# Performance work log

Measured on AMD Instinct MI355X. Metric: run time of the kernel, lower is better.

The kernel has to match this reference:

```python
import jax, jax.numpy as jnp
import numpy as np

N_NODES = 50000
N_EDGES = 640000
RAW = 128
HID = 256
COORD = 3


def setup_inputs() -> dict:
    key = jax.random.key(0)
    ks = jax.random.split(key, 20)

    def w(k, fan_in, fan_out):
        return (jax.random.normal(k, (fan_in, fan_out), jnp.float32)
                / np.float32(np.sqrt(fan_in)))

    return {
        "edge_index": jax.random.randint(ks[0], (2, N_EDGES), 0, N_NODES, jnp.int64)
        if jax.config.jax_enable_x64 else
        jax.random.randint(ks[0], (2, N_EDGES), 0, N_NODES, jnp.int32),
        "str_feature": jax.random.normal(ks[1], (N_NODES, RAW), jnp.float32),
        "coord_feature": jax.random.normal(ks[2], (N_NODES, COORD), jnp.float32),
        # msg_mlp: Linear(2*RAW+1 -> HID), SiLU, Linear(HID -> HID), SiLU
        "msg_w1": w(ks[3], 2 * RAW + 1, HID), "msg_b1": jnp.zeros((HID,), jnp.float32),
        "msg_w2": w(ks[4], HID, HID), "msg_b2": jnp.zeros((HID,), jnp.float32),
        # trans_mlp: Linear(HID->HID), SiLU, Linear(HID->HID), SiLU, Linear(HID->1, no bias, xavier gain=0.001)
        "tr_w1": w(ks[5], HID, HID), "tr_b1": jnp.zeros((HID,), jnp.float32),
        "tr_w2": w(ks[6], HID, HID), "tr_b2": jnp.zeros((HID,), jnp.float32),
        "tr_w3": w(ks[7], HID, 1) * np.float32(0.001),
        # posi_mlp: Linear(RAW+HID->HID), SiLU, Linear(HID->RAW)
        "posi_w1": w(ks[8], RAW + HID, HID), "posi_b1": jnp.zeros((HID,), jnp.float32),
        "posi_w2": w(ks[9], HID, RAW), "posi_b2": jnp.zeros((RAW,), jnp.float32),
    }


def reference(edge_index, str_feature, coord_feature,
              msg_w1, msg_b1, msg_w2, msg_b2,
              tr_w1, tr_b1, tr_w2, tr_b2, tr_w3,
              posi_w1, posi_b1, posi_w2, posi_b2):
    silu = jax.nn.silu
    row, col = edge_index[0], edge_index[1]
    n = str_feature.shape[0]

    # coord2dist
    coord_diff = coord_feature[row] - coord_feature[col]          # [E, 3]
    sqr_dist = jnp.sum(coord_diff * coord_diff, axis=1, keepdims=True)  # [E, 1]

    # msg_model
    edge_in = jnp.concatenate([str_feature[row], str_feature[col], sqr_dist], axis=1)
    msg = silu(silu(edge_in @ msg_w1 + msg_b1) @ msg_w2 + msg_b2)  # [E, HID]

    # coord_model: trans = coord_diff * trans_mlp(msg); x += segment_mean(trans, row)
    gate = silu(silu(msg @ tr_w1 + tr_b1) @ tr_w2 + tr_b2) @ tr_w3  # [E, 1]
    trans = coord_diff * gate                                       # [E, 3]
    trans_sum = jax.ops.segment_sum(trans, row, num_segments=n)     # [N, 3]
    cnt = jax.ops.segment_sum(jnp.ones((trans.shape[0],), trans.dtype), row,
                              num_segments=n)
    trans_mean = trans_sum / jnp.clip(cnt, 1.0)[:, None]
    coord_out = coord_feature + trans_mean

    # posi_model: p + posi_mlp([p, segment_sum(msg, row)])
    msg_sum = jax.ops.segment_sum(msg, row, num_segments=n)         # [N, HID]
    p_in = jnp.concatenate([str_feature, msg_sum], axis=1)
    str_out = str_feature + (silu(p_in @ posi_w1 + posi_b1) @ posi_w2 + posi_b2)

    return str_out, coord_out
```

## Files before the change

kernel.cpp:

```cpp
#include <hip/hip_runtime.h>

#define NN 50000
#define NE 640000

typedef __bf16 bf16x8 __attribute__((ext_vector_type(8)));
typedef short  short8 __attribute__((ext_vector_type(8)));
typedef float  f32x16 __attribute__((ext_vector_type(16)));
typedef float  f32x2  __attribute__((ext_vector_type(2)));
typedef float  f32x4  __attribute__((ext_vector_type(4)));

__device__ __forceinline__ short f2bf(float v) {
  unsigned u = __builtin_bit_cast(unsigned, v);
  u = (u + 0x7FFFu + ((u >> 16) & 1u)) >> 16;
  return (short)u;
}
__device__ __forceinline__ short f2bf_hw(float v) {
  return __builtin_bit_cast(short, (__bf16)v);
}
__device__ __forceinline__ unsigned pack2(float a, float b) {
  return (unsigned)(unsigned short)f2bf_hw(a) | ((unsigned)(unsigned short)f2bf_hw(b) << 16);
}
__device__ __forceinline__ float silu_f(float v) {
  float e = __builtin_amdgcn_exp2f(v * -1.44269504f);
  return v * __builtin_amdgcn_rcpf(1.0f + e);
}
__device__ __forceinline__ bf16x8 ld8(const short* p) {
  return *(const bf16x8*)(p);
}
__device__ __forceinline__ void atomic_add_f(float* p, float v) {
  __hip_atomic_fetch_add(p, v, __ATOMIC_RELAXED, __HIP_MEMORY_SCOPE_AGENT);
}

__global__ void egcl_prep(const float* __restrict__ mw1, const float* __restrict__ mb1,
                          const float* __restrict__ mw2, const float* __restrict__ mb2,
                          const float* __restrict__ tw1, const float* __restrict__ tb1,
                          const float* __restrict__ tw2, const float* __restrict__ tb2,
                          const float* __restrict__ pw1, const float* __restrict__ pw2,
                          const float* __restrict__ strf, const int* __restrict__ rowp,
                          short* __restrict__ w1t, short* __restrict__ w2t,
                          short* __restrict__ t1t, short* __restrict__ t2t,
                          short* __restrict__ p1t, short* __restrict__ p2t,
                          short* __restrict__ strb, int* __restrict__ deg)
{
  const int S0 = 71680, S2 = 98304, S3 = 32768, SS = NN * 128;
  const int total = 4 * S0 + S2 + S3 + SS + NE;
  int stride = gridDim.x * blockDim.x;
  for (int i = blockIdx.x * blockDim.x + threadIdx.x; i < total; i += stride) {
    int j = i;
    if (j < S0) { int n = j / 280, k = j - n * 280;
      float v = (k < 257) ? mw1[k * 256 + n] : ((k == 257) ? mb1[n] : 0.0f);
      w1t[j] = f2bf(v); continue; }
    j -= S0;
    if (j < S0) { int n = j / 280, k = j - n * 280;
      float v = (k < 256) ? mw2[k * 256 + n] : ((k == 257) ? mb2[n] : 0.0f);
      w2t[j] = f2bf(v); continue; }
    j -= S0;
    if (j < S0) { int n = j / 280, k = j - n * 280;
      float v = (k < 256) ? tw1[k * 256 + n] : ((k == 257) ? tb1[n] : 0.0f);
      t1t[j] = f2bf(v); continue; }
    j -= S0;
    if (j < S0) { int n = j / 280, k = j - n * 280;
      float v = (k < 256) ? tw2[k * 256 + n] : ((k == 257) ? tb2[n] : 0.0f);
      t2t[j] = f2bf(v); continue; }
    j -= S0;
    if (j < S2) { int n = j / 384, k = j - n * 384; p1t[j] = f2bf(pw1[k * 256 + n]); continue; }
    j -= S2;
    if (j < S3) { int n = j >> 8, k = j & 255; p2t[j] = f2bf(pw2[k * 128 + n]); continue; }
    j -= S3;
    if (j < SS) { strb[j] = f2bf(strf[j]); continue; }
    j -= SS;
    atomicAdd(deg + rowp[j], 1);
  }
}

__global__ __launch_bounds__(1024)
void egcl_scan(const int* __restrict__ deg, int* __restrict__ base)
{
  __shared__ int wsum[16], wincl[16];
  __shared__ int carry_s;
  const int tid = threadIdx.x, lane = tid & 63, w = tid >> 6;
  if (tid == 0) carry_s = 0;
  __syncthreads();
  for (int start = 0; start < NN; start += 1024) {
    const int i = start + tid;
    int v = (i < NN) ? deg[i] : 0;
    int s = v;
#pragma unroll
    for (int off = 1; off < 64; off <<= 1) {
      int t = __shfl_up(s, off);
      if (lane >= off) s += t;
    }
    if (lane == 63) wsum[w] = s;
    __syncthreads();
    if (w == 0) {
      int u = (lane < 16) ? wsum[lane] : 0;
#pragma unroll
      for (int off = 1; off < 16; off <<= 1) {
        int t = __shfl_up(u, off);
        if (lane >= off) u += t;
      }
      if (lane < 16) wincl[lane] = u;
    }
    __syncthreads();
    const int waveoff = wincl[w] - wsum[w];
    const int carry = carry_s;
    if (i < NN) base[i] = carry + waveoff + s - v;
    __syncthreads();
    if (tid == 0) carry_s = carry + wincl[15];
    __syncthreads();
  }
  if (tid == 0) base[NN] = NE;
}

__global__ void egcl_scatter(const int* __restrict__ rowp, const int* __restrict__ base,
                             int* __restrict__ cursor, int* __restrict__ eidg)
{
  int stride = gridDim.x * blockDim.x;
  for (int e = blockIdx.x * blockDim.x + threadIdx.x; e < NE; e += stride) {
    int r = rowp[e];
    int pos = base[r] + atomicAdd(cursor + r, 1);
    eidg[pos] = e;
  }
}


__device__ __forceinline__ void gemm32(const short* Ab, const short* __restrict__ WT,
                                       int wn, int nh, int lh, int l32,
                                       f32x16 acc[2])
{
  acc[0] = (f32x16)(0.0f); acc[1] = (f32x16)(0.0f);
  const short* arow = Ab + l32 * 280 + lh * 8;
  const short* brow = WT + (wn * 64 + nh * 32 + l32) * 280 + lh * 8;
#pragma unroll
  for (int ks = 0; ks < 17; ++ks) {
    const int kb = ks * 16;
    bf16x8 b  = ld8(brow + kb);
    bf16x8 a0 = ld8(arow + kb);
    bf16x8 a1 = ld8(arow + 32 * 280 + kb);
    acc[0] = __builtin_amdgcn_mfma_f32_32x32x16_bf16(a0, b, acc[0], 0, 0, 0);
    acc[1] = __builtin_amdgcn_mfma_f32_32x32x16_bf16(a1, b, acc[1], 0, 0, 0);
  }
}

__device__ __forceinline__ void comp_pack32(const f32x16 acc[2], unsigned pk[16])
{
#pragma unroll
  for (int sm = 0; sm < 2; ++sm)
#pragma unroll
    for (int j = 0; j < 8; ++j) {
      float v0 = silu_f(acc[sm][2 * j]);
      float v1 = silu_f(acc[sm][2 * j + 1]);
      pk[sm * 8 + j] = pack2(v0, v1);
    }
}

__device__ __forceinline__ void write_pk32(short* Ab, const unsigned pk0[16],
                                           const unsigned pk1[16],
                                           int wn, int lh, int l32)
{
#pragma unroll
  for (int nh = 0; nh < 2; ++nh) {
    const unsigned* pk = nh ? pk1 : pk0;
    const int n = wn * 64 + nh * 32 + l32;
#pragma unroll
    for (int sm = 0; sm < 2; ++sm) {
      short* dst = Ab + (sm * 32 + 4 * lh) * 280 + n;
#pragma unroll
      for (int j = 0; j < 8; ++j) {
        const int row = (j & 1) * 2 + 8 * (j >> 1);
        const unsigned u = pk[sm * 8 + j];
        dst[row * 280]       = (short)(u & 0xFFFFu);
        dst[(row + 1) * 280] = (short)(u >> 16);
      }
    }
  }
}

__global__ __launch_bounds__(256, 4)
void egcl_edge(const int* __restrict__ eidx, const float* __restrict__ coord,
               const short* __restrict__ strb, const int* __restrict__ eidg,
               const int* __restrict__ base,
               const short* __restrict__ w1t, const short* __restrict__ w2t,
               const short* __restrict__ t1t, const short* __restrict__ t2t,
               const float* __restrict__ tr_w3,
               float* __restrict__ msg_sum, float* __restrict__ trans_sum)
{
  __shared__ short Ab[64 * 280];
  __shared__ int   rs_s[64], cs_s[64], own_s[64];
  __shared__ float cdx_s[64], cdy_s[64], cdz_s[64], gate_s[64];

  const int tid  = threadIdx.x;
  const int lane = tid & 63, wave = tid >> 6;
  const int lh = lane >> 5, l32 = lane & 31;
  const int wn = wave;
  const int p0 = blockIdx.x * 64;
  const int* __restrict__ rowp = eidx;
  const int* __restrict__ colp = eidx + NE;

  if (tid < 64) {
    int e = eidg[p0 + tid];
    int r = rowp[e], c = colp[e];
    rs_s[tid] = r; cs_s[tid] = c;
    const int wstart = p0 + (tid & ~31);
    own_s[tid] = (base[r] >= wstart) && (base[r + 1] <= wstart + 32) ? 1 : 0;
    float dx = coord[r * 3 + 0] - coord[c * 3 + 0];
    float dy = coord[r * 3 + 1] - coord[c * 3 + 1];
    float dz = coord[r * 3 + 2] - coord[c * 3 + 2];
    cdx_s[tid] = dx; cdy_s[tid] = dy; cdz_s[tid] = dz;
    short8 d8 = (short8)(short)0;
    d8[0] = f2bf(dx * dx + dy * dy + dz * dz);
    d8[1] = f2bf(1.0f);
    *(short8*)(Ab + tid * 280 + 256) = d8;
    *(short8*)(Ab + tid * 280 + 264) = (short8)(short)0;
    *(short8*)(Ab + tid * 280 + 272) = (short8)(short)0;
  }
  __syncthreads();
#pragma unroll
  for (int it = 0; it < 8; ++it) {
    int i = tid + it * 256;
    int e = i >> 5, cc = i & 31;
    int node = (cc < 16) ? rs_s[e] : cs_s[e];
    short8 v = *(const short8*)(strb + node * 128 + (cc & 15) * 8);
    *(short8*)(Ab + e * 280 + cc * 8) = v;
  }
  __syncthreads();

  f32x16 acc[2];
  unsigned pk0[16], pk1[16];

  gemm32(Ab, w1t, wn, 0, lh, l32, acc);
  comp_pack32(acc, pk0);
  gemm32(Ab, w1t, wn, 1, lh, l32, acc);
  comp_pack32(acc, pk1);
  __syncthreads();
  write_pk32(Ab, pk0, pk1, wn, lh, l32);
  __syncthreads();

  gemm32(Ab, w2t, wn, 0, lh, l32, acc);
  comp_pack32(acc, pk0);
  gemm32(Ab, w2t, wn, 1, lh, l32, acc);
  comp_pack32(acc, pk1);
  __syncthreads();
  write_pk32(Ab, pk0, pk1, wn, lh, l32);
  __syncthreads();

  gemm32(Ab, t1t, wn, 0, lh, l32, acc);
  comp_pack32(acc, pk0);
  gemm32(Ab, t1t, wn, 1, lh, l32, acc);
  comp_pack32(acc, pk1);
  {
    const int cp  = tid & 127;
    const int e0w = (tid >> 7) * 32;
    float run0 = 0.0f, run1 = 0.0f;
    int prev = rs_s[e0w];
    int own  = own_s[e0w];
#pragma unroll 4
    for (int i = 0; i < 32; ++i) {
      const int idx = e0w + i;
      const int r = rs_s[idx];
      unsigned u = *(const unsigned*)(Ab + idx * 280 + cp * 2);
      float lo = __builtin_bit_cast(float, u << 16);
      float hi = __builtin_bit_cast(float, u & 0xFFFF0000u);
      if (r != prev) {
        if (own) {
          f32x2 v; v.x = run0; v.y = run1;
          *((f32x2*)msg_sum + prev * 128 + cp) = v;
        } else {
          atomic_add_f(msg_sum + prev * 256 + cp * 2 + 0, run0);
          atomic_add_f(msg_sum + prev * 256 + cp * 2 + 1, run1);
        }
        run0 = 0.0f; run1 = 0.0f; prev = r; own = own_s[idx];
      }
      run0 += lo; run1 += hi;
    }
    if (own) {
      f32x2 v; v.x = run0; v.y = run1;
      *((f32x2*)msg_sum + prev * 128 + cp) = v;
    } else {
      atomic_add_f(msg_sum + prev * 256 + cp * 2 + 0, run0);
      atomic_add_f(msg_sum + prev * 256 + cp * 2 + 1, run1);
    }
  }
  __syncthreads();
  write_pk32(Ab, pk0, pk1, wn, lh, l32);
  __syncthreads();

  gemm32(Ab, t2t, wn, 0, lh, l32, acc);
  comp_pack32(acc, pk0);
  gemm32(Ab, t2t, wn, 1, lh, l32, acc);
  comp_pack32(acc, pk1);
  __syncthreads();
  write_pk32(Ab, pk0, pk1, wn, lh, l32);
  __syncthreads();

  {
    const int e = tid >> 2, p = tid & 3;
    const short* ap = Ab + e * 280 + p * 64;
    const float4* wp = (const float4*)(tr_w3 + p * 64);
    float s = 0.0f;
#pragma unroll
    for (int j = 0; j < 8; ++j) {
      bf16x8 av = ld8(ap + j * 8);
      float4 w0 = wp[2 * j], w1 = wp[2 * j + 1];
      s += (float)av[0] * w0.x + (float)av[1] * w0.y + (float)av[2] * w0.z + (float)av[3] * w0.w;
      s += (float)av[4] * w1.x + (float)av[5] * w1.y + (float)av[6] * w1.z + (float)av[7] * w1.w;
    }
    s += __shfl_xor(s, 1);
    s += __shfl_xor(s, 2);
    if (p == 0) gate_s[e] = s;
  }
  __syncthreads();
  if (tid < 3) {
    const int c = tid;
    float run = 0.0f;
    int prev = rs_s[0];
    for (int i = 0; i < 64; ++i) {
      const int r = rs_s[i];
      if (r != prev) { atomic_add_f(trans_sum + prev * 3 + c, run); run = 0.0f; prev = r; }
      const float cd = (c == 0) ? cdx_s[i] : ((c == 1) ? cdy_s[i] : cdz_s[i]);
      run += cd * gate_s[i];
    }
    atomic_add_f(trans_sum + prev * 3 + c, run);
  }
}

__global__ __launch_bounds__(256, 3)
void egcl_node(const float* __restrict__ strf, const float* __restrict__ coord,
               const short* __restrict__ strb,
               const short* __restrict__ p1t, const short* __restrict__ p2t,
               const float* __restrict__ pb1, const float* __restrict__ pb2,
               const float* __restrict__ msg_sum, const float* __restrict__ trans_sum,
               const int* __restrict__ base, float* __restrict__ out)
{
  __shared__ short Ab[64 * 392];
  const int tid  = threadIdx.x;
  const int lane = tid & 63, wave = tid >> 6;
  const int quad = lane >> 4, l16 = lane & 15;
  const int n0 = blockIdx.x * 64;

#pragma unroll
  for (int it = 0; it < 4; ++it) {
    int i = tid + it * 256;
    int m = i >> 4, c = i & 15;
    int n = n0 + m;
    short8 v = (short8)(short)0;
    if (n < NN) v = *(const short8*)(strb + n * 128 + c * 8);
    *(short8*)(Ab + m * 392 + c * 8) = v;
  }
#pragma unroll
  for (int it = 0; it < 8; ++it) {
    int i = tid + it * 256;
    int m = i >> 5, c = i & 31;
    int n = n0 + m;
    short8 v = (short8)(short)0;
    if (n < NN) {
      const float* src = msg_sum + n * 256 + c * 8;
#pragma unroll
      for (int j = 0; j < 8; ++j) v[j] = f2bf_hw(src[j]);
    }
    *(short8*)(Ab + m * 392 + 128 + c * 8) = v;
  }
  __syncthreads();

  f32x4 acc[4][4];
#pragma unroll
  for (int nt = 0; nt < 4; ++nt)
#pragma unroll
    for (int mt = 0; mt < 4; ++mt) acc[nt][mt] = (f32x4)(0.0f);
#pragma unroll
  for (int ks = 0; ks < 12; ++ks) {
    const int kb = ks * 32 + quad * 8;
    bf16x8 b[4];
#pragma unroll
    for (int nt = 0; nt < 4; ++nt)
      b[nt] = ld8(p1t + (wave * 64 + nt * 16 + l16) * 384 + kb);
#pragma unroll
    for (int mt = 0; mt < 4; ++mt) {
      bf16x8 a = ld8(Ab + (mt * 16 + l16) * 392 + kb);
#pragma unroll
      for (int nt = 0; nt < 4; ++nt)
        acc[nt][mt] = __builtin_amdgcn_mfma_f32_16x16x32_bf16(a, b[nt], acc[nt][mt], 0, 0, 0);
    }
  }
  __syncthreads();
#pragma unroll
  for (int nt = 0; nt < 4; ++nt) {
    const int n = wave * 64 + nt * 16 + l16;
    const float bn = pb1[n];
#pragma unroll
    for (int mt = 0; mt < 4; ++mt)
#pragma unroll
      for (int r = 0; r < 4; ++r) {
        const int m = mt * 16 + quad * 4 + r;
        Ab[m * 392 + n] = f2bf_hw(silu_f(acc[nt][mt][r] + bn));
      }
  }
  __syncthreads();

  f32x4 a2[2][4];
#pragma unroll
  for (int nt = 0; nt < 2; ++nt)
#pragma unroll
    for (int mt = 0; mt < 4; ++mt) a2[nt][mt] = (f32x4)(0.0f);
#pragma unroll
  for (int ks = 0; ks < 8; ++ks) {
    const int kb = ks * 32 + quad * 8;
    bf16x8 b0 = ld8(p2t + (wave * 32 + l16) * 256 + kb);
    bf16x8 b1 = ld8(p2t + (wave * 32 + 16 + l16) * 256 + kb);
#pragma unroll
    for (int mt = 0; mt < 4; ++mt) {
      bf16x8 a = ld8(Ab + (mt * 16 + l16) * 392 + kb);
      a2[0][mt] = __builtin_amdgcn_mfma_f32_16x16x32_bf16(a, b0, a2[0][mt], 0, 0, 0);
      a2[1][mt] = __builtin_amdgcn_mfma_f32_16x16x32_bf16(a, b1, a2[1][mt], 0, 0, 0);
    }
  }
#pragma unroll
  for (int nt = 0; nt < 2; ++nt) {
    const int c = wave * 32 + nt * 16 + l16;
    const float bc = pb2[c];
#pragma unroll
    for (int mt = 0; mt < 4; ++mt)
#pragma unroll
      for (int r = 0; r < 4; ++r) {
        const int m = mt * 16 + quad * 4 + r;
        const int n = n0 + m;
        if (n < NN) out[n * 128 + c] = strf[n * 128 + c] + a2[nt][mt][r] + bc;
      }
  }
  if (tid < 64) {
    const int n = n0 + tid;
    if (n < NN) {
      float cv = (float)(base[n + 1] - base[n]); if (cv < 1.0f) cv = 1.0f;
      float inv = __builtin_amdgcn_rcpf(cv);
      out[NN * 128 + n * 3 + 0] = coord[n * 3 + 0] + trans_sum[n * 3 + 0] * inv;
      out[NN * 128 + n * 3 + 1] = coord[n * 3 + 1] + trans_sum[n * 3 + 1] * inv;
      out[NN * 128 + n * 3 + 2] = coord[n * 3 + 2] + trans_sum[n * 3 + 2] * inv;
    }
  }
}

extern "C" void kernel_launch(void* const* d_in, const int* in_sizes, int n_in,
                              void* d_out, int out_size, void* d_ws, size_t ws_size,
                              hipStream_t stream)
{
  const int*   eidx   = (const int*)d_in[0];
  const float* strf   = (const float*)d_in[1];
  const float* coord  = (const float*)d_in[2];
  const float* msg_w1 = (const float*)d_in[3];
  const float* msg_b1 = (const float*)d_in[4];
  const float* msg_w2 = (const float*)d_in[5];
  const float* msg_b2 = (const float*)d_in[6];
  const float* tr_w1  = (const float*)d_in[7];
  const float* tr_b1  = (const float*)d_in[8];
  const float* tr_w2  = (const float*)d_in[9];
  const float* tr_b2  = (const float*)d_in[10];
  const float* tr_w3  = (const float*)d_in[11];
  const float* posi_w1 = (const float*)d_in[12];
  const float* posi_b1 = (const float*)d_in[13];
  const float* posi_w2 = (const float*)d_in[14];
  const float* posi_b2 = (const float*)d_in[15];
  float* out = (float*)d_out;

  char* ws = (char*)d_ws;
  float* msg_sum   = (float*)ws;
  float* trans_sum = msg_sum + NN * 256;
  int*   deg       = (int*)(trans_sum + NN * 3);
  int*   cursor    = deg + NN;
  int*   base      = cursor + NN;
  int*   eidg      = base + NN + 8;
  short* strb = (short*)(eidg + NE);
  short* w1t  = strb + NN * 128;
  short* w2t  = w1t + 71680;
  short* t1t  = w2t + 71680;
  short* t2t  = t1t + 71680;
  short* p1t  = t2t + 71680;
  short* p2t  = p1t + 98304;

  const int* rowp = eidx;

  (void)hipMemsetAsync(ws, 0, (size_t)(NN * 256 + NN * 3 + NN + NN) * 4, stream);
  egcl_prep<<<2048, 256, 0, stream>>>(msg_w1, msg_b1, msg_w2, msg_b2,
                                      tr_w1, tr_b1, tr_w2, tr_b2,
                                      posi_w1, posi_w2,
                                      strf, rowp, w1t, w2t, t1t, t2t, p1t, p2t, strb, deg);
  egcl_scan<<<1, 1024, 0, stream>>>(deg, base);
  egcl_scatter<<<2560, 256, 0, stream>>>(rowp, base, cursor, eidg);
  egcl_edge<<<NE / 64, 256, 0, stream>>>(eidx, coord, strb, eidg, base,
                                         w1t, w2t, t1t, t2t, tr_w3,
                                         msg_sum, trans_sum);
  egcl_node<<<(NN + 63) / 64, 256, 0, stream>>>(strf, coord, strb, p1t, p2t,
                                                posi_b1, posi_b2,
                                                msg_sum, trans_sum, base, out);
}
```

Baseline: 976.3 us.

## Compute full 64-column MFMA tiles per wave and fold biases into the epilogue

```diff
diff --git a/kernel.cpp b/kernel.cpp
--- a/kernel.cpp
+++ b/kernel.cpp
@@ -16,9 +16,6 @@
 }
 __device__ __forceinline__ short f2bf_hw(float v) {
   return __builtin_bit_cast(short, (__bf16)v);
-}
-__device__ __forceinline__ unsigned pack2(float a, float b) {
-  return (unsigned)(unsigned short)f2bf_hw(a) | ((unsigned)(unsigned short)f2bf_hw(b) << 16);
 }
 __device__ __forceinline__ float silu_f(float v) {
   float e = __builtin_amdgcn_exp2f(v * -1.44269504f);
@@ -124,53 +121,53 @@
 }
 
 
-__device__ __forceinline__ void gemm32(const short* Ab, const short* __restrict__ WT,
-                                       int wn, int nh, int lh, int l32,
-                                       f32x16 acc[2])
+template<int NKS>
+__device__ __forceinline__ void gemm64(const short* Ab, const short* __restrict__ WT,
+                                       int wn, int lh, int l32, f32x16 acc[4])
 {
   acc[0] = (f32x16)(0.0f); acc[1] = (f32x16)(0.0f);
+  acc[2] = (f32x16)(0.0f); acc[3] = (f32x16)(0.0f);
   const short* arow = Ab + l32 * 280 + lh * 8;
-  const short* brow = WT + (wn * 64 + nh * 32 + l32) * 280 + lh * 8;
-#pragma unroll
-  for (int ks = 0; ks < 17; ++ks) {
+  const short* brow = WT + (wn * 64 + l32) * 280 + lh * 8;
+#pragma unroll
+  for (int ks = 0; ks < NKS; ++ks) {
     const int kb = ks * 16;
-    bf16x8 b  = ld8(brow + kb);
+    bf16x8 b0 = ld8(brow + kb);
+    bf16x8 b1 = ld8(brow + 32 * 280 + kb);
     bf16x8 a0 = ld8(arow + kb);
     bf16x8 a1 = ld8(arow + 32 * 280 + kb);
-    acc[0] = __builtin_amdgcn_mfma_f32_32x32x16_bf16(a0, b, acc[0], 0, 0, 0);
-    acc[1] = __builtin_amdgcn_mfma_f32_32x32x16_bf16(a1, b, acc[1], 0, 0, 0);
-  }
-}
-
-__device__ __forceinline__ void comp_pack32(const f32x16 acc[2], unsigned pk[16])
-{
-#pragma unroll
-  for (int sm = 0; sm < 2; ++sm)
-#pragma unroll
-    for (int j = 0; j < 8; ++j) {
-      float v0 = silu_f(acc[sm][2 * j]);
-      float v1 = silu_f(acc[sm][2 * j + 1]);
-      pk[sm * 8 + j] = pack2(v0, v1);
-    }
-}
-
-__device__ __forceinline__ void write_pk32(short* Ab, const unsigned pk0[16],
-                                           const unsigned pk1[16],
-                                           int wn, int lh, int l32)
+    acc[0] = __builtin_amdgcn_mfma_f32_32x32x16_bf16(a0, b0, acc[0], 0, 0, 0);
+    acc[1] = __builtin_amdgcn_mfma_f32_32x32x16_bf16(a1, b0, acc[1], 0, 0, 0);
+    acc[2] = __builtin_amdgcn_mfma_f32_32x32x16_bf16(a0, b1, acc[2], 0, 0, 0);
+    acc[3] = __builtin_amdgcn_mfma_f32_32x32x16_bf16(a1, b1, acc[3], 0, 0, 0);
+  }
+}
+
+__device__ __forceinline__ void silu_acc(f32x16 acc[4], float b0, float b1)
+{
+#pragma unroll
+  for (int i = 0; i < 4; ++i) {
+    const float b = (i < 2) ? b0 : b1;
+#pragma unroll
+    for (int r = 0; r < 16; ++r) acc[i][r] = silu_f(acc[i][r] + b);
+  }
+}
+
+__device__ __forceinline__ void write_acc(short* Ab, const f32x16 acc[4],
+                                          int wn, int lh, int l32)
 {
 #pragma unroll
   for (int nh = 0; nh < 2; ++nh) {
-    const unsigned* pk = nh ? pk1 : pk0;
     const int n = wn * 64 + nh * 32 + l32;
 #pragma unroll
     for (int sm = 0; sm < 2; ++sm) {
+      const f32x16& a = acc[nh * 2 + sm];
       short* dst = Ab + (sm * 32 + 4 * lh) * 280 + n;
 #pragma unroll
       for (int j = 0; j < 8; ++j) {
         const int row = (j & 1) * 2 + 8 * (j >> 1);
-        const unsigned u = pk[sm * 8 + j];
-        dst[row * 280]       = (short)(u & 0xFFFFu);
-        dst[(row + 1) * 280] = (short)(u >> 16);
+        dst[row * 280]       = f2bf_hw(a[2 * j]);
+        dst[(row + 1) * 280] = f2bf_hw(a[2 * j + 1]);
       }
     }
   }
@@ -182,11 +179,13 @@
                const int* __restrict__ base,
                const short* __restrict__ w1t, const short* __restrict__ w2t,
                const short* __restrict__ t1t, const short* __restrict__ t2t,
+               const float* __restrict__ mb2v, const float* __restrict__ tb1v,
+               const float* __restrict__ tb2v,
                const float* __restrict__ tr_w3,
                float* __restrict__ msg_sum, float* __restrict__ trans_sum)
 {
   __shared__ short Ab[64 * 280];
-  __shared__ int   rs_s[64], cs_s[64], own_s[64];
+  __shared__ int   rs_s[64], own_s[64];
   __shared__ float cdx_s[64], cdy_s[64], cdz_s[64], gate_s[64];
 
   const int tid  = threadIdx.x;
@@ -197,10 +196,15 @@
   const int* __restrict__ rowp = eidx;
   const int* __restrict__ colp = eidx + NE;
 
+  const int nb = wn * 64 + l32;
+  const float b2_0 = mb2v[nb], b2_1 = mb2v[nb + 32];
+  const float b3_0 = tb1v[nb], b3_1 = tb1v[nb + 32];
+  const float b4_0 = tb2v[nb], b4_1 = tb2v[nb + 32];
+
   if (tid < 64) {
     int e = eidg[p0 + tid];
     int r = rowp[e], c = colp[e];
-    rs_s[tid] = r; cs_s[tid] = c;
+    rs_s[tid] = r;
     const int wstart = p0 + (tid & ~31);
     own_s[tid] = (base[r] >= wstart) && (base[r + 1] <= wstart + 32) ? 1 : 0;
     float dx = coord[r * 3 + 0] - coord[c * 3 + 0];
@@ -214,40 +218,33 @@
     *(short8*)(Ab + tid * 280 + 264) = (short8)(short)0;
     *(short8*)(Ab + tid * 280 + 272) = (short8)(short)0;
   }
-  __syncthreads();
 #pragma unroll
   for (int it = 0; it < 8; ++it) {
     int i = tid + it * 256;
     int e = i >> 5, cc = i & 31;
-    int node = (cc < 16) ? rs_s[e] : cs_s[e];
+    int eid = eidg[p0 + e];
+    int node = (cc < 16) ? rowp[eid] : colp[eid];
     short8 v = *(const short8*)(strb + node * 128 + (cc & 15) * 8);
     *(short8*)(Ab + e * 280 + cc * 8) = v;
   }
   __syncthreads();
 
-  f32x16 acc[2];
-  unsigned pk0[16], pk1[16];
-
-  gemm32(Ab, w1t, wn, 0, lh, l32, acc);
-  comp_pack32(acc, pk0);
-  gemm32(Ab, w1t, wn, 1, lh, l32, acc);
-  comp_pack32(acc, pk1);
-  __syncthreads();
-  write_pk32(Ab, pk0, pk1, wn, lh, l32);
-  __syncthreads();
-
-  gemm32(Ab, w2t, wn, 0, lh, l32, acc);
-  comp_pack32(acc, pk0);
-  gemm32(Ab, w2t, wn, 1, lh, l32, acc);
-  comp_pack32(acc, pk1);
-  __syncthreads();
-  write_pk32(Ab, pk0, pk1, wn, lh, l32);
-  __syncthreads();
-
-  gemm32(Ab, t1t, wn, 0, lh, l32, acc);
-  comp_pack32(acc, pk0);
-  gemm32(Ab, t1t, wn, 1, lh, l32, acc);
-  comp_pack32(acc, pk1);
+  f32x16 acc[4];
+
+  gemm64<17>(Ab, w1t, wn, lh, l32, acc);
+  silu_acc(acc, 0.0f, 0.0f);
+  __syncthreads();
+  write_acc(Ab, acc, wn, lh, l32);
+  __syncthreads();
+
+  gemm64<16>(Ab, w2t, wn, lh, l32, acc);
+  silu_acc(acc, b2_0, b2_1);
+  __syncthreads();
+  write_acc(Ab, acc, wn, lh, l32);
+  __syncthreads();
+
+  gemm64<16>(Ab, t1t, wn, lh, l32, acc);
+  silu_acc(acc, b3_0, b3_1);
   {
     const int cp  = tid & 127;
     const int e0w = (tid >> 7) * 32;
@@ -282,15 +279,13 @@
     }
   }
   __syncthreads();
-  write_pk32(Ab, pk0, pk1, wn, lh, l32);
-  __syncthreads();
-
-  gemm32(Ab, t2t, wn, 0, lh, l32, acc);
-  comp_pack32(acc, pk0);
-  gemm32(Ab, t2t, wn, 1, lh, l32, acc);
-  comp_pack32(acc, pk1);
-  __syncthreads();
-  write_pk32(Ab, pk0, pk1, wn, lh, l32);
+  write_acc(Ab, acc, wn, lh, l32);
+  __syncthreads();
+
+  gemm64<16>(Ab, t2t, wn, lh, l32, acc);
+  silu_acc(acc, b4_0, b4_1);
+  __syncthreads();
+  write_acc(Ab, acc, wn, lh, l32);
   __syncthreads();
 
   {
@@ -310,17 +305,24 @@
     if (p == 0) gate_s[e] = s;
   }
   __syncthreads();
-  if (tid < 3) {
-    const int c = tid;
-    float run = 0.0f;
-    int prev = rs_s[0];
-    for (int i = 0; i < 64; ++i) {
-      const int r = rs_s[i];
-      if (r != prev) { atomic_add_f(trans_sum + prev * 3 + c, run); run = 0.0f; prev = r; }
-      const float cd = (c == 0) ? cdx_s[i] : ((c == 1) ? cdy_s[i] : cdz_s[i]);
-      run += cd * gate_s[i];
-    }
-    atomic_add_f(trans_sum + prev * 3 + c, run);
+  if (tid < 64) {
+    const int r = rs_s[tid];
+    const float g = gate_s[tid];
+    float vx = cdx_s[tid] * g, vy = cdy_s[tid] * g, vz = cdz_s[tid] * g;
+#pragma unroll
+    for (int off = 1; off < 64; off <<= 1) {
+      int   rr = __shfl_up(r, off);
+      float tx = __shfl_up(vx, off);
+      float ty = __shfl_up(vy, off);
+      float tz = __shfl_up(vz, off);
+      if (tid >= off && rr == r) { vx += tx; vy += ty; vz += tz; }
+    }
+    int rn = __shfl_down(r, 1);
+    if (tid == 63 || rn != r) {
+      atomic_add_f(trans_sum + r * 3 + 0, vx);
+      atomic_add_f(trans_sum + r * 3 + 1, vy);
+      atomic_add_f(trans_sum + r * 3 + 2, vz);
+    }
   }
 }
 
@@ -486,7 +488,8 @@
   egcl_scan<<<1, 1024, 0, stream>>>(deg, base);
   egcl_scatter<<<2560, 256, 0, stream>>>(rowp, base, cursor, eidg);
   egcl_edge<<<NE / 64, 256, 0, stream>>>(eidx, coord, strb, eidg, base,
-                                         w1t, w2t, t1t, t2t, tr_w3,
+                                         w1t, w2t, t1t, t2t,
+                                         msg_b2, tr_b1, tr_b2, tr_w3,
                                          msg_sum, trans_sum);
   egcl_node<<<(NN + 63) / 64, 256, 0, stream>>>(strf, coord, strb, p1t, p2t,
                                                 posi_b1, posi_b2,
```

Result: slower. 1.040 ms (+6.5%).

## Precompute per-node first-layer projections and gather them per edge

Applied to the files above, without the earlier changes.

```diff
diff --git a/kernel.cpp b/kernel.cpp
--- a/kernel.cpp
+++ b/kernel.cpp
@@ -31,36 +31,35 @@
   __hip_atomic_fetch_add(p, v, __ATOMIC_RELAXED, __HIP_MEMORY_SCOPE_AGENT);
 }
 
-__global__ void egcl_prep(const float* __restrict__ mw1, const float* __restrict__ mb1,
-                          const float* __restrict__ mw2, const float* __restrict__ mb2,
-                          const float* __restrict__ tw1, const float* __restrict__ tb1,
-                          const float* __restrict__ tw2, const float* __restrict__ tb2,
+__global__ void egcl_prep(const float* __restrict__ mw1, const float* __restrict__ mw2,
+                          const float* __restrict__ tw1, const float* __restrict__ tw2,
                           const float* __restrict__ pw1, const float* __restrict__ pw2,
                           const float* __restrict__ strf, const int* __restrict__ rowp,
-                          short* __restrict__ w1t, short* __restrict__ w2t,
+                          short* __restrict__ w1p, short* __restrict__ w2t,
                           short* __restrict__ t1t, short* __restrict__ t2t,
                           short* __restrict__ p1t, short* __restrict__ p2t,
                           short* __restrict__ strb, int* __restrict__ deg)
 {
-  const int S0 = 71680, S2 = 98304, S3 = 32768, SS = NN * 128;
-  const int total = 4 * S0 + S2 + S3 + SS + NE;
+  const int SW1 = 69632, S0 = 71680, S2 = 98304, S3 = 32768, SS = NN * 128;
+  const int total = SW1 + 3 * S0 + S2 + S3 + SS + NE;
   int stride = gridDim.x * blockDim.x;
   for (int i = blockIdx.x * blockDim.x + threadIdx.x; i < total; i += stride) {
     int j = i;
+    if (j < SW1) { int n = j / 136, k = j - n * 136;
+      float v = 0.0f;
+      if (k < 128) v = (n < 256) ? mw1[k * 256 + n] : mw1[(128 + k) * 256 + (n - 256)];
+      w1p[j] = f2bf(v); continue; }
+    j -= SW1;
     if (j < S0) { int n = j / 280, k = j - n * 280;
-      float v = (k < 257) ? mw1[k * 256 + n] : ((k == 257) ? mb1[n] : 0.0f);
-      w1t[j] = f2bf(v); continue; }
-    j -= S0;
-    if (j < S0) { int n = j / 280, k = j - n * 280;
-      float v = (k < 256) ? mw2[k * 256 + n] : ((k == 257) ? mb2[n] : 0.0f);
+      float v = (k < 256) ? mw2[k * 256 + n] : 0.0f;
       w2t[j] = f2bf(v); continue; }
     j -= S0;
     if (j < S0) { int n = j / 280, k = j - n * 280;
-      float v = (k < 256) ? tw1[k * 256 + n] : ((k == 257) ? tb1[n] : 0.0f);
+      float v = (k < 256) ? tw1[k * 256 + n] : 0.0f;
       t1t[j] = f2bf(v); continue; }
     j -= S0;
     if (j < S0) { int n = j / 280, k = j - n * 280;
-      float v = (k < 256) ? tw2[k * 256 + n] : ((k == 257) ? tb2[n] : 0.0f);
+      float v = (k < 256) ? tw2[k * 256 + n] : 0.0f;
       t2t[j] = f2bf(v); continue; }
     j -= S0;
     if (j < S2) { int n = j / 384, k = j - n * 384; p1t[j] = f2bf(pw1[k * 256 + n]); continue; }
@@ -73,6 +72,63 @@
   }
 }
 
+__global__ __launch_bounds__(256)
+void egcl_premlp(const short* __restrict__ strb, const short* __restrict__ w1p,
+                 const float* __restrict__ mb1, float* __restrict__ zab)
+{
+  __shared__ short As[64 * 136];
+  const int tid = threadIdx.x;
+  const int lane = tid & 63, wave = tid >> 6;
+  const int quad = lane >> 4, l16 = lane & 15;
+  const int n0 = blockIdx.x * 64;
+
+  for (int i = tid; i < 64 * 17; i += 256) {
+    int m = i / 17, c = i - m * 17;
+    int n = n0 + m;
+    short8 v = (short8)(short)0;
+    if (c < 16 && n < NN) v = *(const short8*)(strb + n * 128 + c * 8);
+    *(short8*)(As + m * 136 + c * 8) = v;
+  }
+  __syncthreads();
+
+#pragma unroll
+  for (int half = 0; half < 2; ++half) {
+    f32x4 acc[4][4];
+#pragma unroll
+    for (int nt = 0; nt < 4; ++nt)
+#pragma unroll
+      for (int mt = 0; mt < 4; ++mt) acc[nt][mt] = (f32x4)(0.0f);
+#pragma unroll
+    for (int ks = 0; ks < 4; ++ks) {
+      const int kb = ks * 32 + quad * 8;
+      bf16x8 b[4];
+#pragma unroll
+      for (int nt = 0; nt < 4; ++nt)
+        b[nt] = ld8(w1p + (wave * 128 + half * 64 + nt * 16 + l16) * 136 + kb);
+#pragma unroll
+      for (int mt = 0; mt < 4; ++mt) {
+        bf16x8 a = ld8(As + (mt * 16 + l16) * 136 + kb);
+#pragma unroll
+        for (int nt = 0; nt < 4; ++nt)
+          acc[nt][mt] = __builtin_amdgcn_mfma_f32_16x16x32_bf16(a, b[nt], acc[nt][mt], 0, 0, 0);
+      }
+    }
+#pragma unroll
+    for (int nt = 0; nt < 4; ++nt) {
+      const int col = wave * 128 + half * 64 + nt * 16 + l16;
+      const float bias = (col < 256) ? mb1[col] : 0.0f;
+#pragma unroll
+      for (int mt = 0; mt < 4; ++mt)
+#pragma unroll
+        for (int r = 0; r < 4; ++r) {
+          const int m = mt * 16 + quad * 4 + r;
+          const int n = n0 + m;
+          if (n < NN) zab[n * 512 + col] = acc[nt][mt][r] + bias;
+        }
+    }
+  }
+}
+
 __global__ __launch_bounds__(1024)
 void egcl_scan(const int* __restrict__ deg, int* __restrict__ base)
 {
@@ -124,6 +180,7 @@
 }
 
 
+template<int NKS>
 __device__ __forceinline__ void gemm32(const short* Ab, const short* __restrict__ WT,
                                        int wn, int nh, int lh, int l32,
                                        f32x16 acc[2])
@@ -132,7 +189,7 @@
   const short* arow = Ab + l32 * 280 + lh * 8;
   const short* brow = WT + (wn * 64 + nh * 32 + l32) * 280 + lh * 8;
 #pragma unroll
-  for (int ks = 0; ks < 17; ++ks) {
+  for (int ks = 0; ks < NKS; ++ks) {
     const int kb = ks * 16;
     bf16x8 b  = ld8(brow + kb);
     bf16x8 a0 = ld8(arow + kb);
@@ -142,14 +199,14 @@
   }
 }
 
-__device__ __forceinline__ void comp_pack32(const f32x16 acc[2], unsigned pk[16])
+__device__ __forceinline__ void comp_pack32(const f32x16 acc[2], unsigned pk[16], float b)
 {
 #pragma unroll
   for (int sm = 0; sm < 2; ++sm)
 #pragma unroll
     for (int j = 0; j < 8; ++j) {
-      float v0 = silu_f(acc[sm][2 * j]);
-      float v1 = silu_f(acc[sm][2 * j + 1]);
+      float v0 = silu_f(acc[sm][2 * j] + b);
+      float v1 = silu_f(acc[sm][2 * j + 1] + b);
       pk[sm * 8 + j] = pack2(v0, v1);
     }
 }
@@ -178,16 +235,18 @@
 
 __global__ __launch_bounds__(256, 4)
 void egcl_edge(const int* __restrict__ eidx, const float* __restrict__ coord,
-               const short* __restrict__ strb, const int* __restrict__ eidg,
-               const int* __restrict__ base,
-               const short* __restrict__ w1t, const short* __restrict__ w2t,
-               const short* __restrict__ t1t, const short* __restrict__ t2t,
+               const int* __restrict__ eidg, const int* __restrict__ base,
+               const short* __restrict__ w2t, const short* __restrict__ t1t,
+               const short* __restrict__ t2t,
+               const float* __restrict__ mb2v, const float* __restrict__ tb1v,
+               const float* __restrict__ tb2v,
                const float* __restrict__ tr_w3,
+               const float* __restrict__ zab, const float* __restrict__ mw1,
                float* __restrict__ msg_sum, float* __restrict__ trans_sum)
 {
   __shared__ short Ab[64 * 280];
   __shared__ int   rs_s[64], cs_s[64], own_s[64];
-  __shared__ float cdx_s[64], cdy_s[64], cdz_s[64], gate_s[64];
+  __shared__ float cdx_s[64], cdy_s[64], cdz_s[64], dist_s[64], gate_s[64];
 
   const int tid  = threadIdx.x;
   const int lane = tid & 63, wave = tid >> 6;
@@ -196,6 +255,11 @@
   const int p0 = blockIdx.x * 64;
   const int* __restrict__ rowp = eidx;
   const int* __restrict__ colp = eidx + NE;
+
+  const int nb = wn * 64 + l32;
+  const float b2_0 = mb2v[nb], b2_1 = mb2v[nb + 32];
+  const float b3_0 = tb1v[nb], b3_1 = tb1v[nb + 32];
+  const float b4_0 = tb2v[nb], b4_1 = tb2v[nb + 32];
 
   if (tid < 64) {
     int e = eidg[p0 + tid];
@@ -207,47 +271,46 @@
     float dy = coord[r * 3 + 1] - coord[c * 3 + 1];
     float dz = coord[r * 3 + 2] - coord[c * 3 + 2];
     cdx_s[tid] = dx; cdy_s[tid] = dy; cdz_s[tid] = dz;
-    short8 d8 = (short8)(short)0;
-    d8[0] = f2bf(dx * dx + dy * dy + dz * dz);
-    d8[1] = f2bf(1.0f);
-    *(short8*)(Ab + tid * 280 + 256) = d8;
-    *(short8*)(Ab + tid * 280 + 264) = (short8)(short)0;
-    *(short8*)(Ab + tid * 280 + 272) = (short8)(short)0;
-  }
-  __syncthreads();
-#pragma unroll
-  for (int it = 0; it < 8; ++it) {
-    int i = tid + it * 256;
-    int e = i >> 5, cc = i & 31;
-    int node = (cc < 16) ? rs_s[e] : cs_s[e];
-    short8 v = *(const short8*)(strb + node * 128 + (cc & 15) * 8);
-    *(short8*)(Ab + e * 280 + cc * 8) = v;
+    dist_s[tid] = dx * dx + dy * dy + dz * dz;
+  }
+  __syncthreads();
+
+  {
+    const int e = tid >> 2, seg = (tid & 3) * 64;
+    const int r = rs_s[e], c = cs_s[e];
+    const float d = dist_s[e];
+    const float4* za4 = (const float4*)(zab + r * 512 + seg);
+    const float4* zb4 = (const float4*)(zab + c * 512 + 256 + seg);
+    const float4* wd4 = (const float4*)(mw1 + 256 * 256 + seg);
+    short8 hv;
+#pragma unroll
+    for (int j = 0; j < 16; ++j) {
+      float4 a4 = za4[j], b4 = zb4[j], w4 = wd4[j];
+      const int o = (j & 1) * 4;
+      hv[o + 0] = f2bf_hw(silu_f(a4.x + b4.x + d * w4.x));
+      hv[o + 1] = f2bf_hw(silu_f(a4.y + b4.y + d * w4.y));
+      hv[o + 2] = f2bf_hw(silu_f(a4.z + b4.z + d * w4.z));
+      hv[o + 3] = f2bf_hw(silu_f(a4.w + b4.w + d * w4.w));
+      if (j & 1) *(short8*)(Ab + e * 280 + seg + (j - 1) * 4) = hv;
+    }
   }
   __syncthreads();
 
   f32x16 acc[2];
   unsigned pk0[16], pk1[16];
 
-  gemm32(Ab, w1t, wn, 0, lh, l32, acc);
-  comp_pack32(acc, pk0);
-  gemm32(Ab, w1t, wn, 1, lh, l32, acc);
-  comp_pack32(acc, pk1);
+  gemm32<16>(Ab, w2t, wn, 0, lh, l32, acc);
+  comp_pack32(acc, pk0, b2_0);
+  gemm32<16>(Ab, w2t, wn, 1, lh, l32, acc);
+  comp_pack32(acc, pk1, b2_1);
   __syncthreads();
   write_pk32(Ab, pk0, pk1, wn, lh, l32);
   __syncthreads();
 
-  gemm32(Ab, w2t, wn, 0, lh, l32, acc);
-  comp_pack32(acc, pk0);
-  gemm32(Ab, w2t, wn, 1, lh, l32, acc);
-  comp_pack32(acc, pk1);
-  __syncthreads();
-  write_pk32(Ab, pk0, pk1, wn, lh, l32);
-  __syncthreads();
-
-  gemm32(Ab, t1t, wn, 0, lh, l32, acc);
-  comp_pack32(acc, pk0);
-  gemm32(Ab, t1t, wn, 1, lh, l32, acc);
-  comp_pack32(acc, pk1);
+  gemm32<16>(Ab, t1t, wn, 0, lh, l32, acc);
+  comp_pack32(acc, pk0, b3_0);
+  gemm32<16>(Ab, t1t, wn, 1, lh, l32, acc);
+  comp_pack32(acc, pk1, b3_1);
   {
     const int cp  = tid & 127;
     const int e0w = (tid >> 7) * 32;
@@ -285,10 +348,10 @@
   write_pk32(Ab, pk0, pk1, wn, lh, l32);
   __syncthreads();
 
-  gemm32(Ab, t2t, wn, 0, lh, l32, acc);
-  comp_pack32(acc, pk0);
-  gemm32(Ab, t2t, wn, 1, lh, l32, acc);
-  comp_pack32(acc, pk1);
+  gemm32<16>(Ab, t2t, wn, 0, lh, l32, acc);
+  comp_pack32(acc, pk0, b4_0);
+  gemm32<16>(Ab, t2t, wn, 1, lh, l32, acc);
+  comp_pack32(acc, pk1, b4_1);
   __syncthreads();
   write_pk32(Ab, pk0, pk1, wn, lh, l32);
   __syncthreads();
@@ -310,17 +373,24 @@
     if (p == 0) gate_s[e] = s;
   }
   __syncthreads();
-  if (tid < 3) {
-    const int c = tid;
-    float run = 0.0f;
-    int prev = rs_s[0];
-    for (int i = 0; i < 64; ++i) {
-      const int r = rs_s[i];
-      if (r != prev) { atomic_add_f(trans_sum + prev * 3 + c, run); run = 0.0f; prev = r; }
-      const float cd = (c == 0) ? cdx_s[i] : ((c == 1) ? cdy_s[i] : cdz_s[i]);
-      run += cd * gate_s[i];
-    }
-    atomic_add_f(trans_sum + prev * 3 + c, run);
+  if (tid < 64) {
+    const int r = rs_s[tid];
+    const float g = gate_s[tid];
+    float vx = cdx_s[tid] * g, vy = cdy_s[tid] * g, vz = cdz_s[tid] * g;
+#pragma unroll
+    for (int off = 1; off < 64; off <<= 1) {
+      int   rr = __shfl_up(r, off);
+      float tx = __shfl_up(vx, off);
+      float ty = __shfl_up(vy, off);
+      float tz = __shfl_up(vz, off);
+      if (tid >= off && rr == r) { vx += tx; vy += ty; vz += tz; }
+    }
+    int rn = __shfl_down(r, 1);
+    if (tid == 63 || rn != r) {
+      atomic_add_f(trans_sum + r * 3 + 0, vx);
+      atomic_add_f(trans_sum + r * 3 + 1, vy);
+      atomic_add_f(trans_sum + r * 3 + 2, vz);
+    }
   }
 }
 
@@ -469,24 +539,27 @@
   int*   base      = cursor + NN;
   int*   eidg      = base + NN + 8;
   short* strb = (short*)(eidg + NE);
-  short* w1t  = strb + NN * 128;
-  short* w2t  = w1t + 71680;
+  short* w1p  = strb + NN * 128;
+  short* w2t  = w1p + 69632;
   short* t1t  = w2t + 71680;
   short* t2t  = t1t + 71680;
   short* p1t  = t2t + 71680;
   short* p2t  = p1t + 98304;
+  float* zab  = (float*)(p2t + 32768);
 
   const int* rowp = eidx;
 
   (void)hipMemsetAsync(ws, 0, (size_t)(NN * 256 + NN * 3 + NN + NN) * 4, stream);
-  egcl_prep<<<2048, 256, 0, stream>>>(msg_w1, msg_b1, msg_w2, msg_b2,
-                                      tr_w1, tr_b1, tr_w2, tr_b2,
+  egcl_prep<<<2048, 256, 0, stream>>>(msg_w1, msg_w2, tr_w1, tr_w2,
                                       posi_w1, posi_w2,
-                                      strf, rowp, w1t, w2t, t1t, t2t, p1t, p2t, strb, deg);
+                                      strf, rowp, w1p, w2t, t1t, t2t, p1t, p2t, strb, deg);
+  egcl_premlp<<<(NN + 63) / 64, 256, 0, stream>>>(strb, w1p, msg_b1, zab);
   egcl_scan<<<1, 1024, 0, stream>>>(deg, base);
   egcl_scatter<<<2560, 256, 0, stream>>>(rowp, base, cursor, eidg);
-  egcl_edge<<<NE / 64, 256, 0, stream>>>(eidx, coord, strb, eidg, base,
-                                         w1t, w2t, t1t, t2t, tr_w3,
+  egcl_edge<<<NE / 64, 256, 0, stream>>>(eidx, coord, eidg, base,
+                                         w2t, t1t, t2t,
+                                         msg_b2, tr_b1, tr_b2, tr_w3,
+                                         zab, msg_w1,
                                          msg_sum, trans_sum);
   egcl_node<<<(NN + 63) / 64, 256, 0, stream>>>(strf, coord, strb, p1t, p2t,
                                                 posi_b1, posi_b2,
```

Result: slower. 1.084 ms (+11.0%).

## Fuse final gate projection into GEMM epilogue, move biases to registers, parallelize scan

Applied to the files above, without the earlier changes.

```diff
diff --git a/kernel.cpp b/kernel.cpp
--- a/kernel.cpp
+++ b/kernel.cpp
@@ -32,9 +32,8 @@
 }
 
 __global__ void egcl_prep(const float* __restrict__ mw1, const float* __restrict__ mb1,
-                          const float* __restrict__ mw2, const float* __restrict__ mb2,
-                          const float* __restrict__ tw1, const float* __restrict__ tb1,
-                          const float* __restrict__ tw2, const float* __restrict__ tb2,
+                          const float* __restrict__ mw2,
+                          const float* __restrict__ tw1, const float* __restrict__ tw2,
                           const float* __restrict__ pw1, const float* __restrict__ pw2,
                           const float* __restrict__ strf, const int* __restrict__ rowp,
                           short* __restrict__ w1t, short* __restrict__ w2t,
@@ -52,15 +51,15 @@
       w1t[j] = f2bf(v); continue; }
     j -= S0;
     if (j < S0) { int n = j / 280, k = j - n * 280;
-      float v = (k < 256) ? mw2[k * 256 + n] : ((k == 257) ? mb2[n] : 0.0f);
+      float v = (k < 256) ? mw2[k * 256 + n] : 0.0f;
       w2t[j] = f2bf(v); continue; }
     j -= S0;
     if (j < S0) { int n = j / 280, k = j - n * 280;
-      float v = (k < 256) ? tw1[k * 256 + n] : ((k == 257) ? tb1[n] : 0.0f);
+      float v = (k < 256) ? tw1[k * 256 + n] : 0.0f;
       t1t[j] = f2bf(v); continue; }
     j -= S0;
     if (j < S0) { int n = j / 280, k = j - n * 280;
-      float v = (k < 256) ? tw2[k * 256 + n] : ((k == 257) ? tb2[n] : 0.0f);
+      float v = (k < 256) ? tw2[k * 256 + n] : 0.0f;
       t2t[j] = f2bf(v); continue; }
     j -= S0;
     if (j < S2) { int n = j / 384, k = j - n * 384; p1t[j] = f2bf(pw1[k * 256 + n]); continue; }
@@ -77,37 +76,37 @@
 void egcl_scan(const int* __restrict__ deg, int* __restrict__ base)
 {
   __shared__ int wsum[16], wincl[16];
-  __shared__ int carry_s;
   const int tid = threadIdx.x, lane = tid & 63, w = tid >> 6;
-  if (tid == 0) carry_s = 0;
-  __syncthreads();
-  for (int start = 0; start < NN; start += 1024) {
-    const int i = start + tid;
-    int v = (i < NN) ? deg[i] : 0;
-    int s = v;
-#pragma unroll
-    for (int off = 1; off < 64; off <<= 1) {
-      int t = __shfl_up(s, off);
-      if (lane >= off) s += t;
-    }
-    if (lane == 63) wsum[w] = s;
-    __syncthreads();
-    if (w == 0) {
-      int u = (lane < 16) ? wsum[lane] : 0;
-#pragma unroll
-      for (int off = 1; off < 16; off <<= 1) {
-        int t = __shfl_up(u, off);
-        if (lane >= off) u += t;
-      }
-      if (lane < 16) wincl[lane] = u;
-    }
-    __syncthreads();
-    const int waveoff = wincl[w] - wsum[w];
-    const int carry = carry_s;
-    if (i < NN) base[i] = carry + waveoff + s - v;
-    __syncthreads();
-    if (tid == 0) carry_s = carry + wincl[15];
-    __syncthreads();
+  const int i0 = tid * 49;
+  int s = 0;
+#pragma unroll 7
+  for (int k = 0; k < 49; ++k) {
+    int i = i0 + k;
+    if (i < NN) s += deg[i];
+  }
+  int incl = s;
+#pragma unroll
+  for (int off = 1; off < 64; off <<= 1) {
+    int t = __shfl_up(incl, off);
+    if (lane >= off) incl += t;
+  }
+  if (lane == 63) wsum[w] = incl;
+  __syncthreads();
+  if (w == 0) {
+    int u = (lane < 16) ? wsum[lane] : 0;
+#pragma unroll
+    for (int off = 1; off < 16; off <<= 1) {
+      int t = __shfl_up(u, off);
+      if (lane >= off) u += t;
+    }
+    if (lane < 16) wincl[lane] = u;
+  }
+  __syncthreads();
+  int run = (wincl[w] - wsum[w]) + (incl - s);
+#pragma unroll 7
+  for (int k = 0; k < 49; ++k) {
+    int i = i0 + k;
+    if (i < NN) { base[i] = run; run += deg[i]; }
   }
   if (tid == 0) base[NN] = NE;
 }
@@ -124,6 +123,7 @@
 }
 
 
+template<int NKS>
 __device__ __forceinline__ void gemm32(const short* Ab, const short* __restrict__ WT,
                                        int wn, int nh, int lh, int l32,
                                        f32x16 acc[2])
@@ -132,7 +132,7 @@
   const short* arow = Ab + l32 * 280 + lh * 8;
   const short* brow = WT + (wn * 64 + nh * 32 + l32) * 280 + lh * 8;
 #pragma unroll
-  for (int ks = 0; ks < 17; ++ks) {
+  for (int ks = 0; ks < NKS; ++ks) {
     const int kb = ks * 16;
     bf16x8 b  = ld8(brow + kb);
     bf16x8 a0 = ld8(arow + kb);
@@ -142,14 +142,14 @@
   }
 }
 
-__device__ __forceinline__ void comp_pack32(const f32x16 acc[2], unsigned pk[16])
+__device__ __forceinline__ void comp_pack32(const f32x16 acc[2], unsigned pk[16], float b)
 {
 #pragma unroll
   for (int sm = 0; sm < 2; ++sm)
 #pragma unroll
     for (int j = 0; j < 8; ++j) {
-      float v0 = silu_f(acc[sm][2 * j]);
-      float v1 = silu_f(acc[sm][2 * j + 1]);
+      float v0 = silu_f(acc[sm][2 * j] + b);
+      float v1 = silu_f(acc[sm][2 * j + 1] + b);
       pk[sm * 8 + j] = pack2(v0, v1);
     }
 }
@@ -182,6 +182,8 @@
                const int* __restrict__ base,
                const short* __restrict__ w1t, const short* __restrict__ w2t,
                const short* __restrict__ t1t, const short* __restrict__ t2t,
+               const float* __restrict__ mb2v, const float* __restrict__ tb1v,
+               const float* __restrict__ tb2v,
                const float* __restrict__ tr_w3,
                float* __restrict__ msg_sum, float* __restrict__ trans_sum)
 {
@@ -196,6 +198,12 @@
   const int p0 = blockIdx.x * 64;
   const int* __restrict__ rowp = eidx;
   const int* __restrict__ colp = eidx + NE;
+
+  const int nb = wn * 64 + l32;
+  const float b2_0 = mb2v[nb], b2_1 = mb2v[nb + 32];
+  const float b3_0 = tb1v[nb], b3_1 = tb1v[nb + 32];
+  const float b4_0 = tb2v[nb], b4_1 = tb2v[nb + 32];
+  const float w3c0 = tr_w3[nb], w3c1 = tr_w3[nb + 32];
 
   if (tid < 64) {
     int e = eidg[p0 + tid];
@@ -228,26 +236,26 @@
   f32x16 acc[2];
   unsigned pk0[16], pk1[16];
 
-  gemm32(Ab, w1t, wn, 0, lh, l32, acc);
-  comp_pack32(acc, pk0);
-  gemm32(Ab, w1t, wn, 1, lh, l32, acc);
-  comp_pack32(acc, pk1);
+  gemm32<17>(Ab, w1t, wn, 0, lh, l32, acc);
+  comp_pack32(acc, pk0, 0.0f);
+  gemm32<17>(Ab, w1t, wn, 1, lh, l32, acc);
+  comp_pack32(acc, pk1, 0.0f);
   __syncthreads();
   write_pk32(Ab, pk0, pk1, wn, lh, l32);
   __syncthreads();
 
-  gemm32(Ab, w2t, wn, 0, lh, l32, acc);
-  comp_pack32(acc, pk0);
-  gemm32(Ab, w2t, wn, 1, lh, l32, acc);
-  comp_pack32(acc, pk1);
+  gemm32<16>(Ab, w2t, wn, 0, lh, l32, acc);
+  comp_pack32(acc, pk0, b2_0);
+  gemm32<16>(Ab, w2t, wn, 1, lh, l32, acc);
+  comp_pack32(acc, pk1, b2_1);
   __syncthreads();
   write_pk32(Ab, pk0, pk1, wn, lh, l32);
   __syncthreads();
 
-  gemm32(Ab, t1t, wn, 0, lh, l32, acc);
-  comp_pack32(acc, pk0);
-  gemm32(Ab, t1t, wn, 1, lh, l32, acc);
-  comp_pack32(acc, pk1);
+  gemm32<16>(Ab, t1t, wn, 0, lh, l32, acc);
+  comp_pack32(acc, pk0, b3_0);
+  gemm32<16>(Ab, t1t, wn, 1, lh, l32, acc);
+  comp_pack32(acc, pk1, b3_1);
   {
     const int cp  = tid & 127;
     const int e0w = (tid >> 7) * 32;
@@ -285,42 +293,64 @@
   write_pk32(Ab, pk0, pk1, wn, lh, l32);
   __syncthreads();
 
-  gemm32(Ab, t2t, wn, 0, lh, l32, acc);
-  comp_pack32(acc, pk0);
-  gemm32(Ab, t2t, wn, 1, lh, l32, acc);
-  comp_pack32(acc, pk1);
-  __syncthreads();
-  write_pk32(Ab, pk0, pk1, wn, lh, l32);
-  __syncthreads();
-
+  float pd[32];
+  gemm32<16>(Ab, t2t, wn, 0, lh, l32, acc);
+#pragma unroll
+  for (int sm = 0; sm < 2; ++sm)
+#pragma unroll
+    for (int r = 0; r < 16; ++r)
+      pd[sm * 16 + r] = silu_f(acc[sm][r] + b4_0) * w3c0;
+  gemm32<16>(Ab, t2t, wn, 1, lh, l32, acc);
+#pragma unroll
+  for (int sm = 0; sm < 2; ++sm)
+#pragma unroll
+    for (int r = 0; r < 16; ++r)
+      pd[sm * 16 + r] += silu_f(acc[sm][r] + b4_1) * w3c1;
+  __syncthreads();
   {
+    float* AbF = (float*)Ab;
+#pragma unroll
+    for (int sm = 0; sm < 2; ++sm)
+#pragma unroll
+      for (int r = 0; r < 16; ++r) {
+        const int m = (r & 3) + 8 * (r >> 2) + 4 * lh + 32 * sm;
+        AbF[m * 140 + wn * 32 + l32] = pd[sm * 16 + r];
+      }
+  }
+  __syncthreads();
+  {
+    const float* AbF = (const float*)Ab;
     const int e = tid >> 2, p = tid & 3;
-    const short* ap = Ab + e * 280 + p * 64;
-    const float4* wp = (const float4*)(tr_w3 + p * 64);
+    const float* ap = AbF + e * 140 + p * 32;
     float s = 0.0f;
 #pragma unroll
     for (int j = 0; j < 8; ++j) {
-      bf16x8 av = ld8(ap + j * 8);
-      float4 w0 = wp[2 * j], w1 = wp[2 * j + 1];
-      s += (float)av[0] * w0.x + (float)av[1] * w0.y + (float)av[2] * w0.z + (float)av[3] * w0.w;
-      s += (float)av[4] * w1.x + (float)av[5] * w1.y + (float)av[6] * w1.z + (float)av[7] * w1.w;
+      f32x4 v = *(const f32x4*)(ap + j * 4);
+      s += v.x + v.y + v.z + v.w;
     }
     s += __shfl_xor(s, 1);
     s += __shfl_xor(s, 2);
     if (p == 0) gate_s[e] = s;
   }
   __syncthreads();
-  if (tid < 3) {
-    const int c = tid;
-    float run = 0.0f;
-    int prev = rs_s[0];
-    for (int i = 0; i < 64; ++i) {
-      const int r = rs_s[i];
-      if (r != prev) { atomic_add_f(trans_sum + prev * 3 + c, run); run = 0.0f; prev = r; }
-      const float cd = (c == 0) ? cdx_s[i] : ((c == 1) ? cdy_s[i] : cdz_s[i]);
-      run += cd * gate_s[i];
-    }
-    atomic_add_f(trans_sum + prev * 3 + c, run);
+  if (tid < 64) {
+    const int r = rs_s[tid];
+    const float g = gate_s[tid];
+    float vx = cdx_s[tid] * g, vy = cdy_s[tid] * g, vz = cdz_s[tid] * g;
+#pragma unroll
+    for (int off = 1; off < 64; off <<= 1) {
+      int   rr = __shfl_up(r, off);
+      float tx = __shfl_up(vx, off);
+      float ty = __shfl_up(vy, off);
+      float tz = __shfl_up(vz, off);
+      if (tid >= off && rr == r) { vx += tx; vy += ty; vz += tz; }
+    }
+    int rn = __shfl_down(r, 1);
+    if (tid == 63 || rn != r) {
+      atomic_add_f(trans_sum + r * 3 + 0, vx);
+      atomic_add_f(trans_sum + r * 3 + 1, vy);
+      atomic_add_f(trans_sum + r * 3 + 2, vz);
+    }
   }
 }
 
@@ -479,14 +509,15 @@
   const int* rowp = eidx;
 
   (void)hipMemsetAsync(ws, 0, (size_t)(NN * 256 + NN * 3 + NN + NN) * 4, stream);
-  egcl_prep<<<2048, 256, 0, stream>>>(msg_w1, msg_b1, msg_w2, msg_b2,
-                                      tr_w1, tr_b1, tr_w2, tr_b2,
+  egcl_prep<<<2048, 256, 0, stream>>>(msg_w1, msg_b1, msg_w2,
+                                      tr_w1, tr_w2,
                                       posi_w1, posi_w2,
                                       strf, rowp, w1t, w2t, t1t, t2t, p1t, p2t, strb, deg);
   egcl_scan<<<1, 1024, 0, stream>>>(deg, base);
   egcl_scatter<<<2560, 256, 0, stream>>>(rowp, base, cursor, eidg);
   egcl_edge<<<NE / 64, 256, 0, stream>>>(eidx, coord, strb, eidg, base,
-                                         w1t, w2t, t1t, t2t, tr_w3,
+                                         w1t, w2t, t1t, t2t,
+                                         msg_b2, tr_b1, tr_b2, tr_w3,
                                          msg_sum, trans_sum);
   egcl_node<<<(NN + 63) / 64, 256, 0, stream>>>(strf, coord, strb, p1t, p2t,
                                                 posi_b1, posi_b2,
```

After: 1.040 ms. +6.5%, slower.
